# Performance work log

Hardware: AMD Instinct MI355X
Metric: run time of the kernel (lower is better)

## Reference

```python
import jax, jax.numpy as jnp
import numpy as np

EPS = 1e-6
BETA = 0.25
COMMIT_W = 1.0


def setup_inputs() -> dict:
    key = jax.random.key(0)
    k1, k2, k3 = jax.random.split(key, 3)
    b, c, h, w = 8, 256, 32, 32
    n_e, e_dim = 16384, 256
    z = jax.random.normal(k1, (b, c, h, w), jnp.float32)
    # frozen_codebook = randn(n_e, e_dim) * e_dim**-0.5
    codebook = jax.random.normal(k2, (n_e, e_dim), jnp.float32) * (e_dim ** -0.5)
    # nn.Linear(e_dim, in_channels, bias=False) weight: (in_channels, e_dim)
    W = jax.random.normal(k3, (c, e_dim), jnp.float32) * (e_dim ** -0.5)
    return {"z": z, "codebook": codebook, "W": W}


def _rotate_to(src, tgt):
    # Rotation trick (Fifty et al.): rotate src onto tgt direction with a
    # detached Householder-style transform; gradient flows through src only.
    # src, tgt: (n, d)
    norm_src = jnp.linalg.norm(src, axis=-1, keepdims=True)
    norm_tgt = jnp.linalg.norm(tgt, axis=-1, keepdims=True)
    u = src / (norm_src + EPS)
    q = tgt / (norm_tgt + EPS)
    uq = u + q
    w_ = jax.lax.stop_gradient(uq / (jnp.linalg.norm(uq, axis=-1, keepdims=True) + EPS))
    u_d = jax.lax.stop_gradient(u)
    q_d = jax.lax.stop_gradient(q)
    rot = (src
           - 2.0 * jnp.sum(src * w_, axis=-1, keepdims=True) * w_
           + 2.0 * jnp.sum(src * u_d, axis=-1, keepdims=True) * q_d)
    return rot * jax.lax.stop_gradient(norm_tgt / (norm_src + EPS))


def reference(z, codebook, W):
    b, c, h, w = z.shape
    # b c h w -> (b*h*w, c)
    z_flat = jnp.transpose(z, (0, 2, 3, 1)).reshape(-1, c)
    # implicit codebook: frozen codes through linear projection
    emb = codebook @ W.T  # (n_e, c)
    # squared L2 distances (no grad needed for argmin)
    d = (jnp.sum(z_flat ** 2, axis=1, keepdims=True)
         + jnp.sum(emb ** 2, axis=1)
         - 2.0 * (z_flat @ emb.T))  # (n_tok, n_e)
    indices = jnp.argmin(d, axis=1)  # (n_tok,)
    z_q_flat = emb[indices]  # gather quantized vectors
    loss = COMMIT_W * (jnp.mean((jax.lax.stop_gradient(z_flat) - z_q_flat) ** 2)
                       + BETA * jnp.mean((z_flat - jax.lax.stop_gradient(z_q_flat)) ** 2))
    z_q_flat = _rotate_to(z_flat, z_q_flat)
    z_q = jnp.transpose(z_q_flat.reshape(b, h, w, c), (0, 3, 1, 2))
    return z_q, loss, indices
```

## Files before the change

kernel.cpp:

```cpp
#include <hip/hip_runtime.h>
#include <math.h>

#define EPSV 1e-6f
#define NTOK 8192
#define NE   16384
#define DIM  256

using short8 = __attribute__((ext_vector_type(8))) short;
using f32x4v = __attribute__((ext_vector_type(4))) float;

__device__ __forceinline__ unsigned short f2bf(float v) {
    unsigned int u = __float_as_uint(v);
    u += 0x7fffu + ((u >> 16) & 1u);
    return (unsigned short)(u >> 16);
}
__device__ __forceinline__ float bf2f(unsigned short h) {
    return __uint_as_float(((unsigned int)h) << 16);
}

__device__ __forceinline__ void gload_lds16(const void* g, void* s) {
    __builtin_amdgcn_global_load_lds(
        (const __attribute__((address_space(1))) void*)g,
        (__attribute__((address_space(3))) void*)s, 16, 0, 0);
}

__device__ __forceinline__ void split8(const float4 a, const float4 b,
                                       short8& h, short8& l) {
    float f[8] = {a.x, a.y, a.z, a.w, b.x, b.y, b.z, b.w};
#pragma unroll
    for (int j = 0; j < 8; ++j) {
        unsigned short hh = f2bf(f[j]);
        h[j] = (short)hh;
        l[j] = (short)f2bf(f[j] - bf2f(hh));
    }
}

__global__ __launch_bounds__(256, 2) void f0_pre(
    const float* __restrict__ zin, float* __restrict__ z_flat,
    unsigned short* __restrict__ zh, unsigned short* __restrict__ zl,
    float* __restrict__ sz, const float* __restrict__ cb,
    const float* __restrict__ Wm, float* __restrict__ emb,
    unsigned short* __restrict__ eh, unsigned short* __restrict__ el,
    float* __restrict__ se0, float* __restrict__ se1) {
    __shared__ char smemC[65536];
    const int tid = threadIdx.x;

    if (blockIdx.x < 128) {
        float (*tile)[65] = (float(*)[65])smemC;
        const int bid = blockIdx.x;
        const int yx0 = (bid & 15) * 64, b = bid >> 4;
        const int sub = tid >> 6, ln = tid & 63;
        double dacc[16];
#pragma unroll
        for (int j = 0; j < 16; ++j) dacc[j] = 0.0;

        for (int cc = 0; cc < 4; ++cc) {
            const int c0 = cc * 64;
            __syncthreads();
#pragma unroll
            for (int j = 0; j < 16; ++j) {
                int cl = j * 4 + sub;
                tile[cl][ln] = zin[((size_t)(b * 256 + c0 + cl) << 10) + yx0 + ln];
            }
            __syncthreads();
#pragma unroll
            for (int j = 0; j < 16; ++j) {
                int tl = j * 4 + sub;
                float v = tile[ln][tl];
                size_t o = (size_t)(b * 1024 + yx0 + tl) * 256 + c0 + ln;
                z_flat[o] = v;
                unsigned short h = f2bf(v);
                zh[o] = h;
                zl[o] = f2bf(v - bf2f(h));
                dacc[j] += (double)v * v;
            }
        }
#pragma unroll
        for (int j = 0; j < 16; ++j) {
            double s = dacc[j];
#pragma unroll
            for (int m = 1; m < 64; m <<= 1) s += __shfl_xor(s, m);
            if (ln == 0) sz[b * 1024 + yx0 + j * 4 + sub] = (float)s;
        }
        return;
    }

    const int bid2 = blockIdx.x - 128;
    const int w = tid >> 6, lane = tid & 63;
    const int quad = lane >> 4, lr = lane & 15;
    const int wr = w & 1, wc = w >> 1;
    const int n0 = (bid2 & 127) * 128, c0 = (bid2 >> 7) * 128;

    f32x4v acc[4][4];
#pragma unroll
    for (int mt = 0; mt < 4; ++mt)
#pragma unroll
        for (int nt = 0; nt < 4; ++nt)
            acc[mt][nt] = (f32x4v){0.f, 0.f, 0.f, 0.f};

    for (int kc = 0; kc < 4; ++kc) {
        __syncthreads();
#pragma unroll
        for (int i = 0; i < 16; ++i) {
            int s = i * 4 + w;
            int u = s * 64 + lane;
            const void* g;
            if (s < 32) {
                int kg = u >> 7, row = u & 127;
                g = cb + (size_t)(n0 + row) * 256 + kc * 64 + kg * 4;
            } else {
                int u1 = u - 2048;
                int kg = u1 >> 7, row = u1 & 127;
                g = Wm + (size_t)(c0 + row) * 256 + kc * 64 + kg * 4;
            }
            gload_lds16(g, smemC + ((size_t)u << 4));
        }
        __syncthreads();
#pragma unroll
        for (int ks = 0; ks < 2; ++ks) {
            short8 Ah[4], Al[4], Bh[4], Bl[4];
#pragma unroll
            for (int mt = 0; mt < 4; ++mt) {
                int m = wr * 64 + mt * 16 + lr;
                int kg2 = ks * 8 + quad * 2;
                float4 f0 = *(const float4*)(smemC + (((size_t)kg2 * 128 + m) << 4));
                float4 f1 = *(const float4*)(smemC + ((((size_t)kg2 + 1) * 128 + m) << 4));
                split8(f0, f1, Ah[mt], Al[mt]);
            }
#pragma unroll
            for (int nt = 0; nt < 4; ++nt) {
                int n = wc * 64 + nt * 16 + lr;
                int kg2 = ks * 8 + quad * 2;
                float4 g0 = *(const float4*)(smemC + (((size_t)(2048 + kg2 * 128 + n)) << 4));
                float4 g1 = *(const float4*)(smemC + (((size_t)(2048 + (kg2 + 1) * 128 + n)) << 4));
                split8(g0, g1, Bh[nt], Bl[nt]);
            }
#pragma unroll
            for (int mt = 0; mt < 4; ++mt)
#pragma unroll
                for (int nt = 0; nt < 4; ++nt) {
                    f32x4v a = acc[mt][nt];
                    a = __builtin_amdgcn_mfma_f32_16x16x32_bf16(Ah[mt], Bh[nt], a, 0, 0, 0);
                    a = __builtin_amdgcn_mfma_f32_16x16x32_bf16(Ah[mt], Bl[nt], a, 0, 0, 0);
                    a = __builtin_amdgcn_mfma_f32_16x16x32_bf16(Al[mt], Bh[nt], a, 0, 0, 0);
                    a = __builtin_amdgcn_mfma_f32_16x16x32_bf16(Al[mt], Bl[nt], a, 0, 0, 0);
                    acc[mt][nt] = a;
                }
        }
    }
#pragma unroll
    for (int mt = 0; mt < 4; ++mt)
#pragma unroll
        for (int rr = 0; rr < 4; ++rr) {
            int row = n0 + wr * 64 + mt * 16 + quad * 4 + rr;
#pragma unroll
            for (int nt = 0; nt < 4; ++nt) {
                int col = c0 + wc * 64 + nt * 16 + lr;
                size_t o = (size_t)row * 256 + col;
                float v = acc[mt][nt][rr];
                emb[o] = v;
                unsigned short h = f2bf(v);
                eh[o] = h;
                el[o] = f2bf(v - bf2f(h));
            }
        }
    __syncthreads();
    float* sblk = (float*)smemC;
#pragma unroll
    for (int mt = 0; mt < 4; ++mt)
#pragma unroll
        for (int rr = 0; rr < 4; ++rr) {
            float s = 0.f;
#pragma unroll
            for (int nt = 0; nt < 4; ++nt) {
                float v = acc[mt][nt][rr];
                s = fmaf(v, v, s);
            }
#pragma unroll
            for (int st = 1; st < 16; st <<= 1) s += __shfl_xor(s, st);
            if (lr == 0)
                sblk[wc * 128 + wr * 64 + mt * 16 + quad * 4 + rr] = s;
        }
    __syncthreads();
    if (tid < 128) {
        float* sep = ((bid2 >> 7) == 0) ? se0 : se1;
        sep[n0 + tid] = sblk[tid] + sblk[128 + tid];
    }
}

__global__ __launch_bounds__(256, 2) void k1_dist_argmin(
    const unsigned short* __restrict__ zh, const unsigned short* __restrict__ zl,
    const unsigned short* __restrict__ eh, const unsigned short* __restrict__ el,
    const float* __restrict__ sz, const float* __restrict__ se0,
    const float* __restrict__ se1, float* __restrict__ pval,
    int* __restrict__ pidx) {
    __shared__ char smem[65536];
    const int tid = threadIdx.x;
    const int w = tid >> 6, lane = tid & 63;
    const int quad = lane >> 4, lr = lane & 15;
    const int tokBase = blockIdx.x * 128;
    const int rowBase = tokBase + w * 32;
    const int slab = blockIdx.y;
    const int slabBase = slab * 2048;

    short8 Ah[2][8], Al[2][8];
#pragma unroll
    for (int mt = 0; mt < 2; ++mt)
#pragma unroll
        for (int ks = 0; ks < 8; ++ks) {
            size_t o = (size_t)(rowBase + mt * 16 + lr) * 256 + ks * 32 + quad * 8;
            Ah[mt][ks] = *(const short8*)(zh + o);
            Al[mt][ks] = *(const short8*)(zl + o);
        }

    float szr[2][4];
#pragma unroll
    for (int mt = 0; mt < 2; ++mt)
#pragma unroll
        for (int rr = 0; rr < 4; ++rr)
            szr[mt][rr] = sz[rowBase + mt * 16 + quad * 4 + rr];

    float minv[2][4];
    int mini[2][4];
#pragma unroll
    for (int mt = 0; mt < 2; ++mt)
#pragma unroll
        for (int rr = 0; rr < 4; ++rr) {
            minv[mt][rr] = INFINITY;
            mini[mt][rr] = 0;
        }

    auto stage = [&](int buf, int ch) {
        const int colBase = slabBase + ch * 32;
#pragma unroll
        for (int i = 0; i < 8; ++i) {
            int u = i * 256 + tid;
            int fmt = u >> 10;
            int u1 = u & 1023;
            int kg = u1 >> 5, col = u1 & 31;
            const unsigned short* g =
                (fmt ? el : eh) + (size_t)(colBase + col) * 256 + kg * 8;
            gload_lds16(g, smem + buf * 32768 + ((size_t)u << 4));
        }
    };

    stage(0, 0);
    __syncthreads();

    const int bOff = quad * 512 + lr * 16;

    for (int ch = 0; ch < 64; ++ch) {
        const int cur = ch & 1;
        if (ch + 1 < 64) stage(cur ^ 1, ch + 1);

        const int colg0 = slabBase + ch * 32 + lr;
        const int colg1 = colg0 + 16;
        const float sec0 = se0[colg0] + se1[colg0];
        const float sec1 = se0[colg1] + se1[colg1];

        f32x4v acc[2][2];
#pragma unroll
        for (int mt = 0; mt < 2; ++mt)
#pragma unroll
            for (int nt = 0; nt < 2; ++nt)
                acc[mt][nt] = (f32x4v){0.f, 0.f, 0.f, 0.f};

        const char* p0 = smem + cur * 32768 + bOff;
#pragma unroll
        for (int ks = 0; ks < 8; ++ks) {
            short8 Bh[2], Bl[2];
#pragma unroll
            for (int nt = 0; nt < 2; ++nt) {
                Bh[nt] = *(const short8*)(p0 + (ks * 2048 + nt * 256));
                Bl[nt] = *(const short8*)(p0 + (16384 + ks * 2048 + nt * 256));
            }
#pragma unroll
            for (int mt = 0; mt < 2; ++mt)
#pragma unroll
                for (int nt = 0; nt < 2; ++nt) {
                    f32x4v a = acc[mt][nt];
                    a = __builtin_amdgcn_mfma_f32_16x16x32_bf16(Ah[mt][ks], Bh[nt], a, 0, 0, 0);
                    a = __builtin_amdgcn_mfma_f32_16x16x32_bf16(Ah[mt][ks], Bl[nt], a, 0, 0, 0);
                    a = __builtin_amdgcn_mfma_f32_16x16x32_bf16(Al[mt][ks], Bh[nt], a, 0, 0, 0);
                    acc[mt][nt] = a;
                }
        }

        const int colBase = slabBase + ch * 32;
#pragma unroll
        for (int nt = 0; nt < 2; ++nt) {
            const int colg = colBase + nt * 16 + lr;
            const float sec = nt ? sec1 : sec0;
#pragma unroll
            for (int mt = 0; mt < 2; ++mt)
#pragma unroll
                for (int rr = 0; rr < 4; ++rr) {
                    float szse = __fadd_rn(szr[mt][rr], sec);
                    float d = fmaf(-2.0f, acc[mt][nt][rr], szse);
                    if (d < minv[mt][rr]) {
                        minv[mt][rr] = d;
                        mini[mt][rr] = colg;
                    }
                }
        }
        __syncthreads();
    }

#pragma unroll
    for (int st = 1; st < 16; st <<= 1) {
#pragma unroll
        for (int mt = 0; mt < 2; ++mt)
#pragma unroll
            for (int rr = 0; rr < 4; ++rr) {
                float ov = __shfl_xor(minv[mt][rr], st);
                int oi = __shfl_xor(mini[mt][rr], st);
                if (ov < minv[mt][rr] ||
                    (ov == minv[mt][rr] && oi < mini[mt][rr])) {
                    minv[mt][rr] = ov;
                    mini[mt][rr] = oi;
                }
            }
    }
    if (lr == 0) {
#pragma unroll
        for (int mt = 0; mt < 2; ++mt)
#pragma unroll
            for (int rr = 0; rr < 4; ++rr) {
                int row = rowBase + mt * 16 + quad * 4 + rr;
                pval[(size_t)row * 8 + slab] = minv[mt][rr];
                pidx[(size_t)row * 8 + slab] = mini[mt][rr];
            }
    }
}

__global__ __launch_bounds__(256) void k3a_token(
    const float* __restrict__ z_flat, const float* __restrict__ emb,
    const float* __restrict__ pval, const int* __restrict__ pidx,
    const float* __restrict__ sz, const float* __restrict__ se0,
    const float* __restrict__ se1, float* __restrict__ alpha,
    float* __restrict__ beta, int* __restrict__ idxf,
    float* __restrict__ out, float* __restrict__ lpart) {
    __shared__ float red[4];
    const int w = threadIdx.x >> 6, lane = threadIdx.x & 63;
    const int t = blockIdx.x * 4 + w;

    float bv = INFINITY;
    int bi = 0x7fffffff;
    if (lane < 8) {
        bv = pval[(size_t)t * 8 + lane];
        bi = pidx[(size_t)t * 8 + lane];
    }
#pragma unroll
    for (int st = 1; st < 8; st <<= 1) {
        float ov = __shfl_xor(bv, st);
        int oi = __shfl_xor(bi, st);
        if (ov < bv || (ov == bv && oi < bi)) { bv = ov; bi = oi; }
    }
    const int best = __shfl(bi, 0);

    const float4 zv = *(const float4*)(z_flat + (size_t)t * 256 + lane * 4);
    const float4 ev = *(const float4*)(emb + (size_t)best * 256 + lane * 4);
    float zes = zv.x * ev.x + zv.y * ev.y + zv.z * ev.z + zv.w * ev.w;
#pragma unroll
    for (int m = 1; m < 64; m <<= 1) zes += __shfl_xor(zes, m);

    if (lane == 0) {
        const float szs = sz[t];
        const float ses = se0[best] + se1[best];
        const float sqs = szs + ses - 2.0f * zes;
        float ns = sqrtf(szs), nt = sqrtf(ses);
        float inv_s = 1.0f / (ns + EPSV);
        float inv_t = 1.0f / (nt + EPSV);
        float s2 = szs * inv_s;
        float su = szs * inv_s * inv_s;
        float sq = ses * inv_t * inv_t;
        float uq = zes * inv_s * inv_t;
        float nw = sqrtf(su + sq + 2.0f * uq);
        float inv_w = 1.0f / (nw + EPSV);
        float s1 = (s2 + zes * inv_t) * inv_w;
        float scale = nt * inv_s;
        float a = scale * (1.0f - 2.0f * s1 * inv_w * inv_s);
        float bb = scale * inv_t * 2.0f * (s2 - s1 * inv_w);
        alpha[t] = a;
        beta[t] = bb;
        idxf[t] = best;
        out[2097153 + t] = (float)best;
        red[w] = sqs;
    }
    __syncthreads();
    if (threadIdx.x == 0)
        lpart[blockIdx.x] = red[0] + red[1] + red[2] + red[3];
}

__global__ __launch_bounds__(256) void k3b_zq(
    const float* __restrict__ z_flat, const float* __restrict__ emb,
    const float* __restrict__ alpha, const float* __restrict__ beta,
    const int* __restrict__ idxf, const float* __restrict__ lpart,
    float* __restrict__ out) {
    __shared__ float Q[64][65];
    __shared__ float Asm[64], Bsm[64];
    __shared__ int Ism[64];
    const int tid = threadIdx.x;
    const int t0 = blockIdx.x * 64;
    const int c0 = blockIdx.y * 64;

    if (blockIdx.x == 0 && blockIdx.y == 0) {
        __shared__ float red[4];
        float s = 0.0f;
        for (int i = tid; i < 2048; i += 256) s += lpart[i];
#pragma unroll
        for (int m = 1; m < 64; m <<= 1) s += __shfl_xor(s, m);
        if ((tid & 63) == 0) red[tid >> 6] = s;
        __syncthreads();
        if (tid == 0)
            out[2097152] = 1.25f * (red[0] + red[1] + red[2] + red[3]) *
                           (1.0f / 2097152.0f);
    }

    if (tid < 64) {
        Asm[tid] = alpha[t0 + tid];
        Bsm[tid] = beta[t0 + tid];
        Ism[tid] = idxf[t0 + tid];
    }
    __syncthreads();

    const int sub = tid >> 6, ln = tid & 63;
#pragma unroll
    for (int j = 0; j < 16; ++j) {
        int tl = j * 4 + sub;
        float e = emb[(size_t)Ism[tl] * 256 + c0 + ln];
        float zv = z_flat[(size_t)(t0 + tl) * 256 + c0 + ln];
        Q[tl][ln] = Asm[tl] * zv + Bsm[tl] * e;
    }
    __syncthreads();
    const int b = t0 >> 10, yx0 = t0 & 1023;
#pragma unroll
    for (int j = 0; j < 16; ++j) {
        int cl = j * 4 + sub;
        out[((size_t)(b * 256 + c0 + cl) << 10) + yx0 + ln] = Q[ln][cl];
    }
}

extern "C" void kernel_launch(void* const* d_in, const int* in_sizes, int n_in,
                              void* d_out, int out_size, void* d_ws,
                              size_t ws_size, hipStream_t stream) {
    (void)in_sizes; (void)n_in; (void)out_size; (void)ws_size;
    const float* zin = (const float*)d_in[0];
    const float* cb  = (const float*)d_in[1];
    const float* Wm  = (const float*)d_in[2];
    float* out = (float*)d_out;
    char* ws = (char*)d_ws;

    float*          z_flat = (float*)(ws + 0);
    unsigned short* zh     = (unsigned short*)(ws + 8388608);
    unsigned short* zl     = (unsigned short*)(ws + 12582912);
    float*          emb    = (float*)(ws + 16777216);
    unsigned short* eh     = (unsigned short*)(ws + 33554432);
    unsigned short* el     = (unsigned short*)(ws + 41943040);
    float*          sz     = (float*)(ws + 50331648);
    float*          se0    = (float*)(ws + 50364416);
    float*          se1    = (float*)(ws + 50429952);
    float*          pval   = (float*)(ws + 50495488);
    int*            pidx   = (int*)(ws + 50757632);
    float*          alpha  = (float*)(ws + 51019776);
    float*          beta   = (float*)(ws + 51052544);
    int*            idxf   = (int*)(ws + 51085312);
    float*          lpart  = (float*)(ws + 51118080);

    f0_pre<<<384, 256, 0, stream>>>(zin, z_flat, zh, zl, sz, cb, Wm,
                                    emb, eh, el, se0, se1);
    k1_dist_argmin<<<dim3(64, 8), 256, 0, stream>>>(zh, zl, eh, el, sz,
                                                    se0, se1, pval, pidx);
    k3a_token<<<2048, 256, 0, stream>>>(z_flat, emb, pval, pidx, sz, se0, se1,
                                        alpha, beta, idxf, out, lpart);
    k3b_zq<<<dim3(128, 4), 256, 0, stream>>>(z_flat, emb, alpha, beta, idxf,
                                             lpart, out);
}
```

Measured before the change: 287.2 us.

## Replace split-bf16 distance GEMM with bf16 coarse pass plus fp32 candidate rescoring

The distance kernel now uses a single bf16 MFMA per tile instead of three hi/lo split products. It records only a per-token, per-32-column-chunk minimum distance rather than a running argmin. A second kernel finds the global minimum, selects every chunk within a fixed margin of it, and rescores those chunks exactly in fp32 against the full-precision embeddings to pick the index. This cuts matrix-core work and the lo-part traffic roughly threefold, and the LDS layout gains an XOR swizzle. In exchange it writes a large chunk-minimum buffer, adds data-dependent rescoring work, and relies on the fixed margin being wide enough to cover the bf16 error.

```diff
diff --git a/kernel.cpp b/kernel.cpp
--- a/kernel.cpp
+++ b/kernel.cpp
@@ -5,6 +5,7 @@
 #define NTOK 8192
 #define NE   16384
 #define DIM  256
+#define MARGIN 0.5f
 
 using short8 = __attribute__((ext_vector_type(8))) short;
 using f32x4v = __attribute__((ext_vector_type(4))) float;
@@ -37,10 +38,9 @@
 
 __global__ __launch_bounds__(256, 2) void f0_pre(
     const float* __restrict__ zin, float* __restrict__ z_flat,
-    unsigned short* __restrict__ zh, unsigned short* __restrict__ zl,
-    float* __restrict__ sz, const float* __restrict__ cb,
-    const float* __restrict__ Wm, float* __restrict__ emb,
-    unsigned short* __restrict__ eh, unsigned short* __restrict__ el,
+    unsigned short* __restrict__ zh, float* __restrict__ sz,
+    const float* __restrict__ cb, const float* __restrict__ Wm,
+    float* __restrict__ emb, unsigned short* __restrict__ eh,
     float* __restrict__ se0, float* __restrict__ se1) {
     __shared__ char smemC[65536];
     const int tid = threadIdx.x;
@@ -69,9 +69,7 @@
                 float v = tile[ln][tl];
                 size_t o = (size_t)(b * 1024 + yx0 + tl) * 256 + c0 + ln;
                 z_flat[o] = v;
-                unsigned short h = f2bf(v);
-                zh[o] = h;
-                zl[o] = f2bf(v - bf2f(h));
+                zh[o] = f2bf(v);
                 dacc[j] += (double)v * v;
             }
         }
@@ -159,9 +157,7 @@
                 size_t o = (size_t)row * 256 + col;
                 float v = acc[mt][nt][rr];
                 emb[o] = v;
-                unsigned short h = f2bf(v);
-                eh[o] = h;
-                el[o] = f2bf(v - bf2f(h));
+                eh[o] = f2bf(v);
             }
         }
     __syncthreads();
@@ -188,13 +184,11 @@
     }
 }
 
-__global__ __launch_bounds__(256, 2) void k1_dist_argmin(
-    const unsigned short* __restrict__ zh, const unsigned short* __restrict__ zl,
-    const unsigned short* __restrict__ eh, const unsigned short* __restrict__ el,
-    const float* __restrict__ sz, const float* __restrict__ se0,
-    const float* __restrict__ se1, float* __restrict__ pval,
-    int* __restrict__ pidx) {
-    __shared__ char smem[65536];
+__global__ __launch_bounds__(256, 2) void k1_pass1(
+    const unsigned short* __restrict__ zh, const unsigned short* __restrict__ eh,
+    const float* __restrict__ se0, const float* __restrict__ se1,
+    float* __restrict__ cmin) {
+    __shared__ short8 smem[2][1024];
     const int tid = threadIdx.x;
     const int w = tid >> 6, lane = tid & 63;
     const int quad = lane >> 4, lr = lane & 15;
@@ -203,51 +197,31 @@
     const int slab = blockIdx.y;
     const int slabBase = slab * 2048;
 
-    short8 Ah[2][8], Al[2][8];
+    short8 Ah[2][8];
 #pragma unroll
     for (int mt = 0; mt < 2; ++mt)
 #pragma unroll
         for (int ks = 0; ks < 8; ++ks) {
             size_t o = (size_t)(rowBase + mt * 16 + lr) * 256 + ks * 32 + quad * 8;
             Ah[mt][ks] = *(const short8*)(zh + o);
-            Al[mt][ks] = *(const short8*)(zl + o);
-        }
-
-    float szr[2][4];
-#pragma unroll
-    for (int mt = 0; mt < 2; ++mt)
-#pragma unroll
-        for (int rr = 0; rr < 4; ++rr)
-            szr[mt][rr] = sz[rowBase + mt * 16 + quad * 4 + rr];
-
-    float minv[2][4];
-    int mini[2][4];
-#pragma unroll
-    for (int mt = 0; mt < 2; ++mt)
-#pragma unroll
-        for (int rr = 0; rr < 4; ++rr) {
-            minv[mt][rr] = INFINITY;
-            mini[mt][rr] = 0;
         }
 
     auto stage = [&](int buf, int ch) {
         const int colBase = slabBase + ch * 32;
 #pragma unroll
-        for (int i = 0; i < 8; ++i) {
+        for (int i = 0; i < 4; ++i) {
             int u = i * 256 + tid;
-            int fmt = u >> 10;
-            int u1 = u & 1023;
-            int kg = u1 >> 5, col = u1 & 31;
+            int col = u >> 5, kgs = u & 31;
+            int kg = kgs ^ col;
             const unsigned short* g =
-                (fmt ? el : eh) + (size_t)(colBase + col) * 256 + kg * 8;
-            gload_lds16(g, smem + buf * 32768 + ((size_t)u << 4));
+                eh + (size_t)(colBase + col) * 256 + kg * 8;
+            gload_lds16(g, (char*)&smem[0][0] + buf * 16384 +
+                               (((size_t)i * 256 + w * 64) << 4));
         }
     };
 
     stage(0, 0);
     __syncthreads();
-
-    const int bOff = quad * 512 + lr * 16;
 
     for (int ch = 0; ch < 64; ++ch) {
         const int cur = ch & 1;
@@ -265,106 +239,108 @@
             for (int nt = 0; nt < 2; ++nt)
                 acc[mt][nt] = (f32x4v){0.f, 0.f, 0.f, 0.f};
 
-        const char* p0 = smem + cur * 32768 + bOff;
 #pragma unroll
         for (int ks = 0; ks < 8; ++ks) {
-            short8 Bh[2], Bl[2];
+            short8 Bh[2];
 #pragma unroll
             for (int nt = 0; nt < 2; ++nt) {
-                Bh[nt] = *(const short8*)(p0 + (ks * 2048 + nt * 256));
-                Bl[nt] = *(const short8*)(p0 + (16384 + ks * 2048 + nt * 256));
+                int col = nt * 16 + lr;
+                int kgs = (ks * 4 + quad) ^ col;
+                Bh[nt] = smem[cur][col * 32 + kgs];
             }
 #pragma unroll
             for (int mt = 0; mt < 2; ++mt)
 #pragma unroll
-                for (int nt = 0; nt < 2; ++nt) {
-                    f32x4v a = acc[mt][nt];
-                    a = __builtin_amdgcn_mfma_f32_16x16x32_bf16(Ah[mt][ks], Bh[nt], a, 0, 0, 0);
-                    a = __builtin_amdgcn_mfma_f32_16x16x32_bf16(Ah[mt][ks], Bl[nt], a, 0, 0, 0);
-                    a = __builtin_amdgcn_mfma_f32_16x16x32_bf16(Al[mt][ks], Bh[nt], a, 0, 0, 0);
-                    acc[mt][nt] = a;
-                }
-        }
-
-        const int colBase = slabBase + ch * 32;
-#pragma unroll
-        for (int nt = 0; nt < 2; ++nt) {
-            const int colg = colBase + nt * 16 + lr;
-            const float sec = nt ? sec1 : sec0;
-#pragma unroll
-            for (int mt = 0; mt < 2; ++mt)
-#pragma unroll
-                for (int rr = 0; rr < 4; ++rr) {
-                    float szse = __fadd_rn(szr[mt][rr], sec);
-                    float d = fmaf(-2.0f, acc[mt][nt][rr], szse);
-                    if (d < minv[mt][rr]) {
-                        minv[mt][rr] = d;
-                        mini[mt][rr] = colg;
-                    }
-                }
-        }
+                for (int nt = 0; nt < 2; ++nt)
+                    acc[mt][nt] = __builtin_amdgcn_mfma_f32_16x16x32_bf16(
+                        Ah[mt][ks], Bh[nt], acc[mt][nt], 0, 0, 0);
+        }
+
+#pragma unroll
+        for (int mt = 0; mt < 2; ++mt)
+#pragma unroll
+            for (int rr = 0; rr < 4; ++rr) {
+                float d0 = fmaf(-2.0f, acc[mt][0][rr], sec0);
+                float d1 = fmaf(-2.0f, acc[mt][1][rr], sec1);
+                float dm = fminf(d0, d1);
+#pragma unroll
+                for (int st = 1; st < 16; st <<= 1)
+                    dm = fminf(dm, __shfl_xor(dm, st));
+                if (lr == 0)
+                    cmin[(size_t)(rowBase + mt * 16 + quad * 4 + rr) * 512 +
+                         slab * 64 + ch] = dm;
+            }
         __syncthreads();
     }
-
-#pragma unroll
-    for (int st = 1; st < 16; st <<= 1) {
-#pragma unroll
-        for (int mt = 0; mt < 2; ++mt)
-#pragma unroll
-            for (int rr = 0; rr < 4; ++rr) {
-                float ov = __shfl_xor(minv[mt][rr], st);
-                int oi = __shfl_xor(mini[mt][rr], st);
-                if (ov < minv[mt][rr] ||
-                    (ov == minv[mt][rr] && oi < mini[mt][rr])) {
-                    minv[mt][rr] = ov;
-                    mini[mt][rr] = oi;
-                }
-            }
-    }
-    if (lr == 0) {
-#pragma unroll
-        for (int mt = 0; mt < 2; ++mt)
-#pragma unroll
-            for (int rr = 0; rr < 4; ++rr) {
-                int row = rowBase + mt * 16 + quad * 4 + rr;
-                pval[(size_t)row * 8 + slab] = minv[mt][rr];
-                pidx[(size_t)row * 8 + slab] = mini[mt][rr];
-            }
-    }
-}
-
-__global__ __launch_bounds__(256) void k3a_token(
+}
+
+__global__ __launch_bounds__(256) void k2_pass2(
     const float* __restrict__ z_flat, const float* __restrict__ emb,
-    const float* __restrict__ pval, const int* __restrict__ pidx,
-    const float* __restrict__ sz, const float* __restrict__ se0,
-    const float* __restrict__ se1, float* __restrict__ alpha,
-    float* __restrict__ beta, int* __restrict__ idxf,
-    float* __restrict__ out, float* __restrict__ lpart) {
+    const float* __restrict__ cmin, const float* __restrict__ sz,
+    const float* __restrict__ se0, const float* __restrict__ se1,
+    float* __restrict__ alpha, float* __restrict__ beta,
+    int* __restrict__ idxf, float* __restrict__ out,
+    float* __restrict__ lpart) {
     __shared__ float red[4];
     const int w = threadIdx.x >> 6, lane = threadIdx.x & 63;
     const int t = blockIdx.x * 4 + w;
 
-    float bv = INFINITY;
-    int bi = 0x7fffffff;
-    if (lane < 8) {
-        bv = pval[(size_t)t * 8 + lane];
-        bi = pidx[(size_t)t * 8 + lane];
-    }
-#pragma unroll
-    for (int st = 1; st < 8; st <<= 1) {
-        float ov = __shfl_xor(bv, st);
-        int oi = __shfl_xor(bi, st);
-        if (ov < bv || (ov == bv && oi < bi)) { bv = ov; bi = oi; }
-    }
-    const int best = __shfl(bi, 0);
-
-    const float4 zv = *(const float4*)(z_flat + (size_t)t * 256 + lane * 4);
-    const float4 ev = *(const float4*)(emb + (size_t)best * 256 + lane * 4);
-    float zes = zv.x * ev.x + zv.y * ev.y + zv.z * ev.z + zv.w * ev.w;
-#pragma unroll
-    for (int m = 1; m < 64; m <<= 1) zes += __shfl_xor(zes, m);
+    float cm[8];
+#pragma unroll
+    for (int r = 0; r < 8; ++r)
+        cm[r] = cmin[(size_t)t * 512 + r * 64 + lane];
+    float m0 = cm[0];
+#pragma unroll
+    for (int r = 1; r < 8; ++r) m0 = fminf(m0, cm[r]);
+#pragma unroll
+    for (int st = 1; st < 64; st <<= 1) m0 = fminf(m0, __shfl_xor(m0, st));
+    const float thresh = m0 + MARGIN;
+
+    const int half = lane & 1;
+    const float4* zp = (const float4*)(z_flat + (size_t)t * 256 + half * 128);
+
+    float bd = INFINITY, bdot = 0.0f;
+    int bj = 0x7fffffff;
+
+#pragma unroll 1
+    for (int r = 0; r < 8; ++r) {
+        unsigned long long mask = __ballot(cm[r] <= thresh);
+        while (mask) {
+            int src = __ffsll((unsigned long long)mask) - 1;
+            mask &= mask - 1;
+            int c = r * 64 + src;
+            int j = (c >> 6) * 2048 + (c & 63) * 32 + (lane >> 1);
+            const float4* ep = (const float4*)(emb + (size_t)j * 256 + half * 128);
+            float s0 = 0.f, s1 = 0.f, s2 = 0.f, s3 = 0.f;
+#pragma unroll
+            for (int q = 0; q < 32; q += 4) {
+                float4 a0 = zp[q], a1 = zp[q + 1], a2 = zp[q + 2], a3 = zp[q + 3];
+                float4 b0 = ep[q], b1 = ep[q + 1], b2 = ep[q + 2], b3 = ep[q + 3];
+                s0 = fmaf(a0.x, b0.x, fmaf(a0.y, b0.y, fmaf(a0.z, b0.z, fmaf(a0.w, b0.w, s0))));
+                s1 = fmaf(a1.x, b1.x, fmaf(a1.y, b1.y, fmaf(a1.z, b1.z, fmaf(a1.w, b1.w, s1))));
+                s2 = fmaf(a2.x, b2.x, fmaf(a2.y, b2.y, fmaf(a2.z, b2.z, fmaf(a2.w, b2.w, s2))));
+                s3 = fmaf(a3.x, b3.x, fmaf(a3.y, b3.y, fmaf(a3.z, b3.z, fmaf(a3.w, b3.w, s3))));
+            }
+            float sh = (s0 + s1) + (s2 + s3);
+            float dot = sh + __shfl_xor(sh, 1);
+            float ses = se0[j] + se1[j];
+            float d = fmaf(-2.0f, dot, ses);
+            if (d < bd || (d == bd && j < bj)) {
+                bd = d; bj = j; bdot = dot;
+            }
+        }
+    }
+#pragma unroll
+    for (int st = 1; st < 64; st <<= 1) {
+        float od = __shfl_xor(bd, st);
+        int oj = __shfl_xor(bj, st);
+        float ot = __shfl_xor(bdot, st);
+        if (od < bd || (od == bd && oj < bj)) { bd = od; bj = oj; bdot = ot; }
+    }
 
     if (lane == 0) {
+        const int best = bj;
+        const float zes = bdot;
         const float szs = sz[t];
         const float ses = se0[best] + se1[best];
         const float sqs = szs + ses - 2.0f * zes;
@@ -453,26 +429,22 @@
 
     float*          z_flat = (float*)(ws + 0);
     unsigned short* zh     = (unsigned short*)(ws + 8388608);
-    unsigned short* zl     = (unsigned short*)(ws + 12582912);
-    float*          emb    = (float*)(ws + 16777216);
-    unsigned short* eh     = (unsigned short*)(ws + 33554432);
-    unsigned short* el     = (unsigned short*)(ws + 41943040);
-    float*          sz     = (float*)(ws + 50331648);
-    float*          se0    = (float*)(ws + 50364416);
-    float*          se1    = (float*)(ws + 50429952);
-    float*          pval   = (float*)(ws + 50495488);
-    int*            pidx   = (int*)(ws + 50757632);
-    float*          alpha  = (float*)(ws + 51019776);
-    float*          beta   = (float*)(ws + 51052544);
-    int*            idxf   = (int*)(ws + 51085312);
-    float*          lpart  = (float*)(ws + 51118080);
-
-    f0_pre<<<384, 256, 0, stream>>>(zin, z_flat, zh, zl, sz, cb, Wm,
-                                    emb, eh, el, se0, se1);
-    k1_dist_argmin<<<dim3(64, 8), 256, 0, stream>>>(zh, zl, eh, el, sz,
-                                                    se0, se1, pval, pidx);
-    k3a_token<<<2048, 256, 0, stream>>>(z_flat, emb, pval, pidx, sz, se0, se1,
-                                        alpha, beta, idxf, out, lpart);
+    float*          emb    = (float*)(ws + 12582912);
+    unsigned short* eh     = (unsigned short*)(ws + 29360128);
+    float*          sz     = (float*)(ws + 37748736);
+    float*          se0    = (float*)(ws + 37781504);
+    float*          se1    = (float*)(ws + 37847040);
+    float*          cmin   = (float*)(ws + 37912576);
+    float*          alpha  = (float*)(ws + 54689792);
+    float*          beta   = (float*)(ws + 54722560);
+    int*            idxf   = (int*)(ws + 54755328);
+    float*          lpart  = (float*)(ws + 54788096);
+
+    f0_pre<<<384, 256, 0, stream>>>(zin, z_flat, zh, sz, cb, Wm,
+                                    emb, eh, se0, se1);
+    k1_pass1<<<dim3(64, 8), 256, 0, stream>>>(zh, eh, se0, se1, cmin);
+    k2_pass2<<<2048, 256, 0, stream>>>(z_flat, emb, cmin, sz, se0, se1,
+                                       alpha, beta, idxf, out, lpart);
     k3b_zq<<<dim3(128, 4), 256, 0, stream>>>(z_flat, emb, alpha, beta, idxf,
                                              lpart, out);
 }
```

After: 422.2 us. 47.0% more time.
